# Optimization experiments

Measured on AMD Instinct MI355X. Metric: run time of the kernel, lower is better.

Reference implementation:

```python
import jax, jax.numpy as jnp
import numpy as np

N, F_IN, F_OUT, P, E = 50000, 64, 64, 8, 800000


def setup_inputs() -> dict:
    key = jax.random.key(0)
    ks = jax.random.split(key, 11)
    s = 0.05
    X = jax.random.normal(ks[0], (N, F_IN, P), jnp.float32)
    edge_index = jax.random.randint(ks[1], (2, E), 0, N)
    edge_weight = jax.random.uniform(ks[2], (E,), jnp.float32)
    # Stacked ChebConv (K=2) params for gates [i, f, c, o]
    Wx0 = jax.random.normal(ks[3], (4, F_IN, F_OUT), jnp.float32) * s
    Wx1 = jax.random.normal(ks[4], (4, F_IN, F_OUT), jnp.float32) * s
    bx = jax.random.normal(ks[5], (4, F_OUT), jnp.float32) * s
    Wh0 = jax.random.normal(ks[6], (4, F_OUT, F_OUT), jnp.float32) * s
    Wh1 = jax.random.normal(ks[7], (4, F_OUT, F_OUT), jnp.float32) * s
    bh = jax.random.normal(ks[8], (4, F_OUT), jnp.float32) * s
    wc = jax.random.normal(ks[9], (3, F_OUT), jnp.float32) * s  # peepholes for i, f, o
    bg = jax.random.normal(ks[10], (4, F_OUT), jnp.float32) * s  # gate biases i, f, c, o
    return dict(X=X, edge_index=edge_index, edge_weight=edge_weight,
                Wx0=Wx0, Wx1=Wx1, bx=bx, Wh0=Wh0, Wh1=Wh1, bh=bh, wc=wc, bg=bg)


def reference(X, edge_index, edge_weight, Wx0, Wx1, bx, Wh0, Wh1, bh, wc, bg):
    src, dst = edge_index[0], edge_index[1]
    # sym-normalized Laplacian, scaled by 2/lambda_max with lambda_max=2, minus I:
    # L_hat = -D^{-1/2} A D^{-1/2}  (diagonal cancels exactly in ChebConv.__norm__)
    deg = jax.ops.segment_sum(edge_weight, src, num_segments=N)
    dis = jnp.where(deg > 0, jax.lax.rsqrt(jnp.maximum(deg, 1e-12)), 0.0)
    wn = -dis[src] * edge_weight * dis[dst]  # [E]

    def cheb(x, W0, W1, b):
        # ChebConv K=2: T0(x)=x, T1(x)=L_hat x ; out = x@W0 + (L_hat x)@W1 + b
        tx1 = jax.ops.segment_sum(wn[:, None] * x[src], dst, num_segments=N)
        return x @ W0 + tx1 @ W1 + b

    def step(Xp):  # one GConvLSTM step from zero hidden/cell state (H=None, C=None)
        H = jnp.zeros((N, F_OUT), X.dtype)
        C = jnp.zeros((N, F_OUT), X.dtype)
        I = jax.nn.sigmoid(cheb(Xp, Wx0[0], Wx1[0], bx[0]) + cheb(H, Wh0[0], Wh1[0], bh[0]) + wc[0] * C + bg[0])
        Fg = jax.nn.sigmoid(cheb(Xp, Wx0[1], Wx1[1], bx[1]) + cheb(H, Wh0[1], Wh1[1], bh[1]) + wc[1] * C + bg[1])
        T = jnp.tanh(cheb(Xp, Wx0[2], Wx1[2], bx[2]) + cheb(H, Wh0[2], Wh1[2], bh[2]) + bg[2])
        Cn = Fg * C + I * T
        O = jax.nn.sigmoid(cheb(Xp, Wx0[3], Wx1[3], bx[3]) + cheb(H, Wh0[3], Wh1[3], bh[3]) + wc[2] * Cn + bg[3])
        return O * jnp.tanh(Cn)

    # periods are independent (fresh zero state each period) -> vmap then sum
    Hs = jax.vmap(step)(jnp.moveaxis(X, 2, 0))  # [P, N, F_OUT]
    return Hs.sum(axis=0)
```

## Files before the change

### kernel.cpp

```cpp
#include <hip/hip_runtime.h>
#include <hip/hip_fp16.h>

#define NN 50000
#define EE 800000
#define FF 64
#define PP 8
#define NPAD 50048
#define ELLW 64

typedef _Float16 half8 __attribute__((ext_vector_type(8)));
typedef _Float16 half4 __attribute__((ext_vector_type(4)));
typedef float floatx4 __attribute__((ext_vector_type(4)));

static constexpr size_t al512(size_t x) { return (x + 511) & ~size_t(511); }
static constexpr size_t OFF_DEG  = 0;
static constexpr size_t OFF_CNT  = al512(OFF_DEG  + (size_t)NN*4);
static constexpr size_t OFF_DIS  = al512(OFF_CNT  + (size_t)NN*4);
static constexpr size_t OFF_ELL  = al512(OFF_DIS  + (size_t)NN*4);
static constexpr size_t OFF_BIAS = al512(OFF_ELL  + (size_t)NN*ELLW*8);
static constexpr size_t OFF_WC2  = al512(OFF_BIAS + 192*4);
static constexpr size_t OFF_WFRG = al512(OFF_WC2  + 64*4);
static constexpr size_t OFF_XB   = al512(OFF_WFRG + (size_t)24576*2);
static constexpr size_t OFF_TB   = al512(OFF_XB   + (size_t)NPAD*512*2);

__global__ void k_build(const int* __restrict__ src, const int* __restrict__ dst,
                        const float* __restrict__ ew,
                        float* __restrict__ deg, int* __restrict__ cnt,
                        int2* __restrict__ ell) {
    int e = blockIdx.x * 256 + threadIdx.x;
    if (e < EE) {
        int s = src[e], d = dst[e];
        float w = ew[e];
        atomicAdd(deg + s, w);
        int pos = atomicAdd(cnt + d, 1);
        if (pos < ELLW) {
            int2 pr; pr.x = s; pr.y = __float_as_int(w);
            ell[(size_t)d * ELLW + pos] = pr;
        }
    }
}

__global__ void k_prep(const float* __restrict__ Wx0, const float* __restrict__ Wx1,
                       const float* __restrict__ bx, const float* __restrict__ bh,
                       const float* __restrict__ wc, const float* __restrict__ bg,
                       const float* __restrict__ deg,
                       _Float16* __restrict__ Wfrag, float* __restrict__ biasv,
                       float* __restrict__ wc2, float* __restrict__ dis) {
    int t = blockIdx.x * 256 + threadIdx.x;
    const int gmap[3] = {0, 2, 3};
    if (t < NN) {
        float dg = deg[t];
        dis[t] = dg > 0.f ? rsqrtf(fmaxf(dg, 1e-12f)) : 0.f;
    }
    if (t < 24576) {
        int j8 = t & 7;
        int lane = (t >> 3) & 63;
        int rem = t >> 9;
        int ct = rem % 12;
        int ks = rem / 12;
        int k = ks * 32 + (lane >> 4) * 8 + j8;
        int gp = ct >> 2;
        int g = gmap[gp];
        int j64 = (ct & 3) * 16 + (lane & 15);
        float val = (k < 64) ? Wx0[((size_t)g * 64 + k) * 64 + j64]
                             : Wx1[((size_t)g * 64 + (k - 64)) * 64 + j64];
        Wfrag[t] = (_Float16)val;
    }
    if (t < 192) {
        int gp = t / 64, j = t % 64;
        int g = gmap[gp];
        biasv[t] = bx[g * 64 + j] + bh[g * 64 + j] + bg[g * 64 + j];
    }
    if (t < 64) wc2[t] = wc[2 * 64 + t];
}

__global__ void k_wfix(const float* __restrict__ dis, const int* __restrict__ cnt,
                       int2* __restrict__ ell) {
    int wid = threadIdx.x >> 6, lane = threadIdx.x & 63;
    int n = blockIdx.x * 4 + wid;
    if (n >= NN) return;
    int cn = min(cnt[n], ELLW);
    if (lane < cn) {
        int2* p = ell + (size_t)n * ELLW + lane;
        int2 ed = *p;
        float w = dis[ed.x] * __int_as_float(ed.y);
        p->y = __float_as_int(w);
    }
}

__global__ void k_xpose(const float* __restrict__ X, _Float16* __restrict__ XB) {
    __shared__ _Float16 tile[4][512];
    int wid = threadIdx.x >> 6, lane = threadIdx.x & 63;
    int n = blockIdx.x * 4 + wid;
    if (n < NN) {
        const float4* xp = (const float4*)(X + (size_t)n * 512 + lane * 8);
        float4 a = xp[0], b = xp[1];
        float v[8] = {a.x, a.y, a.z, a.w, b.x, b.y, b.z, b.w};
#pragma unroll
        for (int p = 0; p < PP; ++p)
            tile[wid][p * 64 + lane] = (_Float16)v[p];
        half8 vv = *(const half8*)&tile[wid][lane * 8];
        *(half8*)(XB + (size_t)n * 512 + lane * 8) = vv;
    }
}

__global__ void k_spmm(const _Float16* __restrict__ XB, const int* __restrict__ cnt,
                       const float* __restrict__ dis, const int2* __restrict__ ell,
                       _Float16* __restrict__ TB) {
    int wid = threadIdx.x >> 6, lane = threadIdx.x & 63;
    int b = blockIdx.x;
    int half = b & 1;
    int n = (b >> 1) * 4 + wid;
    if (n >= NN) return;
    float acc[4] = {0.f, 0.f, 0.f, 0.f};
    int cn = min(cnt[n], ELLW);
    float dn = dis[n];
    const int foff = half * 256 + lane * 4;
    if (cn > 0) {
        const int2* __restrict__ row = ell + (size_t)n * ELLW;
        int2 ed = row[min(lane, cn - 1)];
        int wli = (lane < cn) ? ed.y : 0;
        for (int base = 0; base < cn; base += 16) {
            half4 r[16];
            float wk[16];
#pragma unroll
            for (int u = 0; u < 16; ++u) {
                int srck = __builtin_amdgcn_readlane(ed.x, base + u);
                wk[u] = __int_as_float(__builtin_amdgcn_readlane(wli, base + u));
                r[u] = *(const half4*)(XB + (size_t)srck * 512 + foff);
            }
#pragma unroll
            for (int u = 0; u < 16; ++u) {
#pragma unroll
                for (int j = 0; j < 4; ++j) acc[j] += wk[u] * (float)r[u][j];
            }
        }
    }
    half4 st;
#pragma unroll
    for (int j = 0; j < 4; ++j) st[j] = (_Float16)(-dn * acc[j]);
    *(half4*)(TB + (size_t)n * 512 + foff) = st;
}

__device__ __forceinline__ float fast_rcp(float x) { return __builtin_amdgcn_rcpf(x); }
__device__ __forceinline__ float sigmoidf_fast(float x) {
    return fast_rcp(1.f + __expf(-x));
}
__device__ __forceinline__ float tanhf_fast(float x) {
    return 1.f - 2.f * fast_rcp(1.f + __expf(2.f * x));
}

__global__ __launch_bounds__(256) void k_gemm(const _Float16* __restrict__ XB,
                                              const _Float16* __restrict__ TB,
                                              const _Float16* __restrict__ Wfrag,
                                              const float* __restrict__ biasv,
                                              const float* __restrict__ wc2,
                                              float* __restrict__ out) {
    __shared__ _Float16 Wl[24576];
    const int tid = threadIdx.x;
    const int wid = tid >> 6, lane = tid & 63;
    {
        const half8* __restrict__ Wg = (const half8*)Wfrag;
        half8* Wls = (half8*)Wl;
#pragma unroll
        for (int i = 0; i < 12; ++i) Wls[i * 256 + tid] = Wg[i * 256 + tid];
    }
    __syncthreads();
    const half8* Wl8 = (const half8*)Wl;

    const int n0 = blockIdx.x * 128 + wid * 32;
    const int jj = lane & 15, quad = lane >> 4;

    float bi[4], bc[4], bo[4], wcv[4];
#pragma unroll
    for (int c4 = 0; c4 < 4; ++c4) {
        int j = c4 * 16 + jj;
        bi[c4] = biasv[j];
        bc[c4] = biasv[64 + j];
        bo[c4] = biasv[128 + j];
        wcv[c4] = wc2[j];
    }

    const _Float16* __restrict__ x0 = XB + (size_t)(n0 + jj) * 512;
    const _Float16* __restrict__ x1 = XB + (size_t)(n0 + 16 + jj) * 512;
    const _Float16* __restrict__ t0 = TB + (size_t)(n0 + jj) * 512;
    const _Float16* __restrict__ t1 = TB + (size_t)(n0 + 16 + jj) * 512;

    floatx4 outacc[2][4];
#pragma unroll
    for (int r = 0; r < 2; ++r)
#pragma unroll
        for (int c4 = 0; c4 < 4; ++c4) outacc[r][c4] = (floatx4){0.f, 0.f, 0.f, 0.f};

#pragma unroll 1
    for (int p = 0; p < PP; ++p) {
        const int o = p * 64 + quad * 8;
        half8 a00 = *(const half8*)(x0 + o);
        half8 a01 = *(const half8*)(x0 + o + 32);
        half8 a02 = *(const half8*)(t0 + o);
        half8 a03 = *(const half8*)(t0 + o + 32);
        half8 a10 = *(const half8*)(x1 + o);
        half8 a11 = *(const half8*)(x1 + o + 32);
        half8 a12 = *(const half8*)(t1 + o);
        half8 a13 = *(const half8*)(t1 + o + 32);
#pragma unroll
        for (int c4 = 0; c4 < 4; ++c4) {
            floatx4 ai0 = {0.f,0.f,0.f,0.f}, ac0 = {0.f,0.f,0.f,0.f}, ao0 = {0.f,0.f,0.f,0.f};
            floatx4 ai1 = {0.f,0.f,0.f,0.f}, ac1 = {0.f,0.f,0.f,0.f}, ao1 = {0.f,0.f,0.f,0.f};
#pragma unroll
            for (int ks = 0; ks < 4; ++ks) {
                half8 bfi = Wl8[(ks * 12 + c4) * 64 + lane];
                half8 bfc = Wl8[(ks * 12 + 4 + c4) * 64 + lane];
                half8 bfo = Wl8[(ks * 12 + 8 + c4) * 64 + lane];
                half8 a0 = (ks == 0) ? a00 : (ks == 1) ? a01 : (ks == 2) ? a02 : a03;
                half8 a1 = (ks == 0) ? a10 : (ks == 1) ? a11 : (ks == 2) ? a12 : a13;
                ai0 = __builtin_amdgcn_mfma_f32_16x16x32_f16(a0, bfi, ai0, 0, 0, 0);
                ai1 = __builtin_amdgcn_mfma_f32_16x16x32_f16(a1, bfi, ai1, 0, 0, 0);
                ac0 = __builtin_amdgcn_mfma_f32_16x16x32_f16(a0, bfc, ac0, 0, 0, 0);
                ac1 = __builtin_amdgcn_mfma_f32_16x16x32_f16(a1, bfc, ac1, 0, 0, 0);
                ao0 = __builtin_amdgcn_mfma_f32_16x16x32_f16(a0, bfo, ao0, 0, 0, 0);
                ao1 = __builtin_amdgcn_mfma_f32_16x16x32_f16(a1, bfo, ao1, 0, 0, 0);
            }
#pragma unroll
            for (int rr = 0; rr < 4; ++rr) {
                float I0 = sigmoidf_fast(ai0[rr] + bi[c4]);
                float T0 = tanhf_fast(ac0[rr] + bc[c4]);
                float Cn0 = I0 * T0;
                float O0 = sigmoidf_fast(ao0[rr] + bo[c4] + wcv[c4] * Cn0);
                outacc[0][c4][rr] += O0 * tanhf_fast(Cn0);
                float I1 = sigmoidf_fast(ai1[rr] + bi[c4]);
                float T1 = tanhf_fast(ac1[rr] + bc[c4]);
                float Cn1 = I1 * T1;
                float O1 = sigmoidf_fast(ao1[rr] + bo[c4] + wcv[c4] * Cn1);
                outacc[1][c4][rr] += O1 * tanhf_fast(Cn1);
            }
        }
    }
#pragma unroll
    for (int r = 0; r < 2; ++r)
#pragma unroll
        for (int c4 = 0; c4 < 4; ++c4)
#pragma unroll
            for (int rr = 0; rr < 4; ++rr) {
                int n = n0 + r * 16 + quad * 4 + rr;
                if (n < NN) out[(size_t)n * 64 + c4 * 16 + jj] = outacc[r][c4][rr];
            }
}

extern "C" void kernel_launch(void* const* d_in, const int* in_sizes, int n_in,
                              void* d_out, int out_size, void* d_ws, size_t ws_size,
                              hipStream_t stream) {
    const float* X   = (const float*)d_in[0];
    const int*   ei  = (const int*)d_in[1];
    const float* ew  = (const float*)d_in[2];
    const float* Wx0 = (const float*)d_in[3];
    const float* Wx1 = (const float*)d_in[4];
    const float* bx  = (const float*)d_in[5];
    const float* bh  = (const float*)d_in[8];
    const float* wc  = (const float*)d_in[9];
    const float* bg  = (const float*)d_in[10];
    float* out = (float*)d_out;

    const int* src = ei;
    const int* dst = ei + EE;

    char* ws = (char*)d_ws;
    float* deg     = (float*)(ws + OFF_DEG);
    int*   cnt     = (int*)(ws + OFF_CNT);
    float* dis     = (float*)(ws + OFF_DIS);
    int2*  ell     = (int2*)(ws + OFF_ELL);
    float* biasv   = (float*)(ws + OFF_BIAS);
    float* wc2     = (float*)(ws + OFF_WC2);
    _Float16* Wfrag = (_Float16*)(ws + OFF_WFRG);
    _Float16* XB    = (_Float16*)(ws + OFF_XB);
    _Float16* TB    = (_Float16*)(ws + OFF_TB);

    hipMemsetAsync(ws, 0, OFF_DIS, stream);

    k_build<<<(EE + 255) / 256, 256, 0, stream>>>(src, dst, ew, deg, cnt, ell);
    k_prep<<<196, 256, 0, stream>>>(Wx0, Wx1, bx, bh, wc, bg, deg, Wfrag, biasv, wc2, dis);
    k_wfix<<<(NN + 3) / 4, 256, 0, stream>>>(dis, cnt, ell);
    k_xpose<<<(NN + 3) / 4, 256, 0, stream>>>(X, XB);
    k_spmm<<<2 * ((NN + 3) / 4), 256, 0, stream>>>(XB, cnt, dis, ell, TB);
    k_gemm<<<(NN + 127) / 128, 256, 0, stream>>>(XB, TB, Wfrag, biasv, wc2, out);
}
```

Measured before the change: 454.6 us.

## Fuse wfix with xpose, chunk spmm launches, read GEMM weights from global

Merges the edge-weight fixup and the X transpose/convert into one kernel, saving a launch and a pass over the node grid. SpMM now runs as four launches over node ranges, which may help L2 locality of the gathered rows but adds launch overhead. The GEMM kernel drops its shared-memory weight staging and uses 64-thread blocks that read weight fragments straight from global memory through the cache. This raises block count and occupancy but repeats the weight loads from L2/L1 on every use.

```diff
diff --git a/kernel.cpp b/kernel.cpp
--- a/kernel.cpp
+++ b/kernel.cpp
@@ -74,8 +74,10 @@
     if (t < 64) wc2[t] = wc[2 * 64 + t];
 }
 
-__global__ void k_wfix(const float* __restrict__ dis, const int* __restrict__ cnt,
-                       int2* __restrict__ ell) {
+__global__ void k_xw(const float* __restrict__ X, _Float16* __restrict__ XB,
+                     const float* __restrict__ dis, const int* __restrict__ cnt,
+                     int2* __restrict__ ell) {
+    __shared__ _Float16 tile[4][512];
     int wid = threadIdx.x >> 6, lane = threadIdx.x & 63;
     int n = blockIdx.x * 4 + wid;
     if (n >= NN) return;
@@ -86,32 +88,24 @@
         float w = dis[ed.x] * __int_as_float(ed.y);
         p->y = __float_as_int(w);
     }
-}
-
-__global__ void k_xpose(const float* __restrict__ X, _Float16* __restrict__ XB) {
-    __shared__ _Float16 tile[4][512];
-    int wid = threadIdx.x >> 6, lane = threadIdx.x & 63;
-    int n = blockIdx.x * 4 + wid;
-    if (n < NN) {
-        const float4* xp = (const float4*)(X + (size_t)n * 512 + lane * 8);
-        float4 a = xp[0], b = xp[1];
-        float v[8] = {a.x, a.y, a.z, a.w, b.x, b.y, b.z, b.w};
-#pragma unroll
-        for (int p = 0; p < PP; ++p)
-            tile[wid][p * 64 + lane] = (_Float16)v[p];
-        half8 vv = *(const half8*)&tile[wid][lane * 8];
-        *(half8*)(XB + (size_t)n * 512 + lane * 8) = vv;
-    }
+    const float4* xp = (const float4*)(X + (size_t)n * 512 + lane * 8);
+    float4 a = xp[0], b = xp[1];
+    float v[8] = {a.x, a.y, a.z, a.w, b.x, b.y, b.z, b.w};
+#pragma unroll
+    for (int p = 0; p < PP; ++p)
+        tile[wid][p * 64 + lane] = (_Float16)v[p];
+    half8 vv = *(const half8*)&tile[wid][lane * 8];
+    *(half8*)(XB + (size_t)n * 512 + lane * 8) = vv;
 }
 
 __global__ void k_spmm(const _Float16* __restrict__ XB, const int* __restrict__ cnt,
                        const float* __restrict__ dis, const int2* __restrict__ ell,
-                       _Float16* __restrict__ TB) {
+                       _Float16* __restrict__ TB, int n_base, int n_end) {
     int wid = threadIdx.x >> 6, lane = threadIdx.x & 63;
     int b = blockIdx.x;
     int half = b & 1;
-    int n = (b >> 1) * 4 + wid;
-    if (n >= NN) return;
+    int n = n_base + (b >> 1) * 4 + wid;
+    if (n >= n_end) return;
     float acc[4] = {0.f, 0.f, 0.f, 0.f};
     int cn = min(cnt[n], ELLW);
     float dn = dis[n];
@@ -150,25 +144,16 @@
     return 1.f - 2.f * fast_rcp(1.f + __expf(2.f * x));
 }
 
-__global__ __launch_bounds__(256) void k_gemm(const _Float16* __restrict__ XB,
-                                              const _Float16* __restrict__ TB,
-                                              const _Float16* __restrict__ Wfrag,
-                                              const float* __restrict__ biasv,
-                                              const float* __restrict__ wc2,
-                                              float* __restrict__ out) {
-    __shared__ _Float16 Wl[24576];
-    const int tid = threadIdx.x;
-    const int wid = tid >> 6, lane = tid & 63;
-    {
-        const half8* __restrict__ Wg = (const half8*)Wfrag;
-        half8* Wls = (half8*)Wl;
-#pragma unroll
-        for (int i = 0; i < 12; ++i) Wls[i * 256 + tid] = Wg[i * 256 + tid];
-    }
-    __syncthreads();
-    const half8* Wl8 = (const half8*)Wl;
-
-    const int n0 = blockIdx.x * 128 + wid * 32;
+__global__ __launch_bounds__(64) void k_gemm(const _Float16* __restrict__ XB,
+                                             const _Float16* __restrict__ TB,
+                                             const _Float16* __restrict__ Wfrag,
+                                             const float* __restrict__ biasv,
+                                             const float* __restrict__ wc2,
+                                             float* __restrict__ out) {
+    const int lane = threadIdx.x & 63;
+    const half8* __restrict__ Wg8 = (const half8*)Wfrag;
+
+    const int n0 = blockIdx.x * 32;
     const int jj = lane & 15, quad = lane >> 4;
 
     float bi[4], bc[4], bo[4], wcv[4];
@@ -209,9 +194,9 @@
             floatx4 ai1 = {0.f,0.f,0.f,0.f}, ac1 = {0.f,0.f,0.f,0.f}, ao1 = {0.f,0.f,0.f,0.f};
 #pragma unroll
             for (int ks = 0; ks < 4; ++ks) {
-                half8 bfi = Wl8[(ks * 12 + c4) * 64 + lane];
-                half8 bfc = Wl8[(ks * 12 + 4 + c4) * 64 + lane];
-                half8 bfo = Wl8[(ks * 12 + 8 + c4) * 64 + lane];
+                half8 bfi = Wg8[(ks * 12 + c4) * 64 + lane];
+                half8 bfc = Wg8[(ks * 12 + 4 + c4) * 64 + lane];
+                half8 bfo = Wg8[(ks * 12 + 8 + c4) * 64 + lane];
                 half8 a0 = (ks == 0) ? a00 : (ks == 1) ? a01 : (ks == 2) ? a02 : a03;
                 half8 a1 = (ks == 0) ? a10 : (ks == 1) ? a11 : (ks == 2) ? a12 : a13;
                 ai0 = __builtin_amdgcn_mfma_f32_16x16x32_f16(a0, bfi, ai0, 0, 0, 0);
@@ -279,8 +264,10 @@
 
     k_build<<<(EE + 255) / 256, 256, 0, stream>>>(src, dst, ew, deg, cnt, ell);
     k_prep<<<196, 256, 0, stream>>>(Wx0, Wx1, bx, bh, wc, bg, deg, Wfrag, biasv, wc2, dis);
-    k_wfix<<<(NN + 3) / 4, 256, 0, stream>>>(dis, cnt, ell);
-    k_xpose<<<(NN + 3) / 4, 256, 0, stream>>>(X, XB);
-    k_spmm<<<2 * ((NN + 3) / 4), 256, 0, stream>>>(XB, cnt, dis, ell, TB);
-    k_gemm<<<(NN + 127) / 128, 256, 0, stream>>>(XB, TB, Wfrag, biasv, wc2, out);
-}
+    k_xw<<<(NN + 3) / 4, 256, 0, stream>>>(X, XB, dis, cnt, ell);
+    for (int r = 0; r < 4; ++r) {
+        int nb = r * 12500, ne = min(NN, nb + 12500);
+        k_spmm<<<2 * ((ne - nb + 3) / 4), 256, 0, stream>>>(XB, cnt, dis, ell, TB, nb, ne);
+    }
+    k_gemm<<<NPAD / 32, 64, 0, stream>>>(XB, TB, Wfrag, biasv, wc2, out);
+}
```

New measurement: 461.5 us. Within noise of the previous version (+1.5%).
